# Performance work log

Measured on AMD Instinct MI355X. Metric: run time of the kernel, lower is better.

## Reference

```python
import jax, jax.numpy as jnp
import numpy as np

N_EMBD = 1024
HEAD_SIZE = 64  # n_embd // n_head = 1024 // 16


def setup_inputs() -> dict:
    key = jax.random.key(0)
    ks = jax.random.split(key, 7)
    B, T, C, H = 4, 2048, N_EMBD, HEAD_SIZE
    s = 1.0 / np.sqrt(C)
    return {
        "x": jax.random.normal(ks[0], (B, T, C), dtype=jnp.float32),
        "Wq": jax.random.normal(ks[1], (C, H), dtype=jnp.float32) * s,
        "bq": jax.random.normal(ks[2], (H,), dtype=jnp.float32) * 0.01,
        "Wk": jax.random.normal(ks[3], (C, H), dtype=jnp.float32) * s,
        "bk": jax.random.normal(ks[4], (H,), dtype=jnp.float32) * 0.01,
        "Wv": jax.random.normal(ks[5], (C, H), dtype=jnp.float32) * s,
        "bv": jax.random.normal(ks[6], (H,), dtype=jnp.float32) * 0.01,
    }


def reference(x, Wq, bq, Wk, bk, Wv, bv):
    # x: [B, T, C]
    B, T, C = x.shape
    q = x @ Wq + bq  # [B, T, H]
    k = x @ Wk + bk  # [B, T, H]
    v = x @ Wv + bv  # [B, T, H]
    # NOTE: original module does NOT scale by 1/sqrt(head_size)
    wei = jnp.einsum("bth,bsh->bts", q, k)  # [B, T, T]
    causal = jnp.tril(jnp.ones((T, T), dtype=bool))
    wei = jnp.where(causal, wei, -jnp.inf)
    wei = jax.nn.softmax(wei, axis=-1)
    out = jnp.einsum("bts,bsh->bth", wei, v)  # [B, T, H]
    return out
```

## Files before the change

### kernel.cpp

```cpp
#include <hip/hip_runtime.h>

typedef float f32x4 __attribute__((ext_vector_type(4)));
typedef short s16x4 __attribute__((ext_vector_type(4)));
typedef short s16x8 __attribute__((ext_vector_type(8)));

#define LOG2E 1.4426950408889634f

__device__ __forceinline__ short f2bf(float f) {
  unsigned u = __float_as_uint(f);
  unsigned r = (u + 0x7fffu + ((u >> 16) & 1u)) >> 16;
  return (short)r;
}
__device__ __forceinline__ float bf2f(short s) {
  return __uint_as_float(((unsigned)(unsigned short)s) << 16);
}
__device__ __forceinline__ unsigned cvt_pk_bf16(float a, float b) {
  unsigned r;
  asm("v_cvt_pk_bf16_f32 %0, %1, %2" : "=v"(r) : "v"(a), "v"(b));
  return r;
}

__device__ __forceinline__ f32x4 mfma16(s16x4 a, s16x4 b, f32x4 c) {
  return __builtin_amdgcn_mfma_f32_16x16x16bf16_1k(a, b, c, 0, 0, 0);
}
__device__ __forceinline__ f32x4 mfma32(s16x8 a, s16x8 b, f32x4 c) {
  return __builtin_amdgcn_mfma_f32_16x16x32_bf16(a, b, c, 0, 0, 0);
}

__device__ __forceinline__ void gl_lds16(const void* gp, void* sp) {
  __builtin_amdgcn_global_load_lds(
      (__attribute__((address_space(1))) void*)const_cast<void*>(gp),
      (__attribute__((address_space(3))) void*)sp, 16, 0, 0);
}

__global__ __launch_bounds__(256) void prep_w(
    const float* __restrict__ Wq, const float* __restrict__ Wk, const float* __restrict__ Wv,
    short* __restrict__ wt_hi, short* __restrict__ wt_lo) {
  int idx = blockIdx.x * 256 + threadIdx.x;
  int n = idx >> 10;
  int c = idx & 1023;
  const float* W = (n < 64) ? Wq : ((n < 128) ? Wk : Wv);
  float v = W[c * 64 + (n & 63)];
  short hi = f2bf(v);
  short lo = f2bf(v - bf2f(hi));
  wt_hi[idx] = hi;
  wt_lo[idx] = lo;
}

__global__ __launch_bounds__(512, 2) void proj_qkv(
    const float* __restrict__ x,
    const short* __restrict__ wt_hi, const short* __restrict__ wt_lo,
    const float* __restrict__ bq, const float* __restrict__ bk, const float* __restrict__ bv,
    short* __restrict__ q_hi, short* __restrict__ q_lo,
    short* __restrict__ k_hi, short* __restrict__ k_lo,
    short* __restrict__ v_t) {
  const int tid = threadIdx.x;
  const int lane = tid & 63;
  const int wv = tid >> 6;
  const int col = lane & 15;
  const int g = lane >> 4;
  const int mg = wv >> 2;
  const int ng = wv & 3;
  const int tokbase = blockIdx.x * 32;

  __shared__ short lds[5][12288];

  const int wsl = ((lane & 3) ^ ((lane >> 3) & 3)) * 8;
  const short* s0 = wt_hi + (size_t)(16 * wv + (lane >> 2)) * 1024 + wsl;
  const int d0 = wv * 512;
  const int c1 = wv + 8;
  const short* s1 = (c1 < 12 ? wt_hi + (size_t)(16 * c1 + (lane >> 2)) * 1024
                             : wt_lo + (size_t)(16 * (c1 - 12) + (lane >> 2)) * 1024) + wsl;
  const int d1 = (c1 < 12) ? c1 * 512 : 6144 + (c1 - 12) * 512;
  const int c2 = wv + 16;
  const bool isx = (c2 >= 20);
  const short* s2 = isx
      ? (const short*)(x + (size_t)(tokbase + 8 * (c2 - 20) + (lane >> 3)) * 1024 +
                       ((lane & 7) ^ (lane >> 3)) * 4)
      : wt_lo + (size_t)(16 * (c2 - 12) + (lane >> 2)) * 1024 + wsl;
  const int d2 = isx ? 10240 + (c2 - 20) * 512 : 6144 + (c2 - 12) * 512;
  const int st2 = isx ? 64 : 32;

#define STAGE(BP, S) do { \
    gl_lds16(s0 + (S) * 32, (BP) + d0); \
    gl_lds16(s1 + (S) * 32, (BP) + d1); \
    gl_lds16(s2 + (S) * st2, (BP) + d2); \
  } while (0)

#define PIPE_WAIT(N) do { \
    asm volatile("s_waitcnt vmcnt(" #N ")" ::: "memory"); \
    __builtin_amdgcn_s_barrier(); \
    __builtin_amdgcn_sched_barrier(0); \
  } while (0)
#define PIPE_END do { \
    asm volatile("s_waitcnt lgkmcnt(0)" ::: "memory"); \
    __builtin_amdgcn_sched_barrier(0); \
    __builtin_amdgcn_s_barrier(); \
  } while (0)

  const int arow = mg * 16 + col;
  const int xq0 = ((2 * g) ^ (arow & 7)) << 2;
  const int xq1 = ((2 * g + 1) ^ (arow & 7)) << 2;
  const int rq = ng * 16 + col;
  const int ws = (g ^ ((rq >> 1) & 3)) << 3;

  f32x4 accQ = {0,0,0,0}, accK = {0,0,0,0}, accV = {0,0,0,0};

  typedef union { unsigned u[4]; s16x8 v8; } pk8;

#define COMPUTE(BP) do { \
    const short* bp_ = (BP); \
    const float* xb_ = (const float*)(bp_ + 10240); \
    f32x4 x0_ = *(const f32x4*)(xb_ + arow * 32 + xq0); \
    f32x4 x1_ = *(const f32x4*)(xb_ + arow * 32 + xq1); \
    pk8 xh_, xl_; \
    xh_.u[0] = cvt_pk_bf16(x0_[0], x0_[1]); \
    xh_.u[1] = cvt_pk_bf16(x0_[2], x0_[3]); \
    xh_.u[2] = cvt_pk_bf16(x1_[0], x1_[1]); \
    xh_.u[3] = cvt_pk_bf16(x1_[2], x1_[3]); \
    xl_.u[0] = cvt_pk_bf16(x0_[0] - __uint_as_float(xh_.u[0] << 16), \
                           x0_[1] - __uint_as_float(xh_.u[0] & 0xffff0000u)); \
    xl_.u[1] = cvt_pk_bf16(x0_[2] - __uint_as_float(xh_.u[1] << 16), \
                           x0_[3] - __uint_as_float(xh_.u[1] & 0xffff0000u)); \
    xl_.u[2] = cvt_pk_bf16(x1_[0] - __uint_as_float(xh_.u[2] << 16), \
                           x1_[1] - __uint_as_float(xh_.u[2] & 0xffff0000u)); \
    xl_.u[3] = cvt_pk_bf16(x1_[2] - __uint_as_float(xh_.u[3] << 16), \
                           x1_[3] - __uint_as_float(xh_.u[3] & 0xffff0000u)); \
    s16x8 qh_ = *(const s16x8*)(bp_ + rq * 32 + ws); \
    s16x8 kh_ = *(const s16x8*)(bp_ + (64 + rq) * 32 + ws); \
    s16x8 vh_ = *(const s16x8*)(bp_ + (128 + rq) * 32 + ws); \
    s16x8 ql_ = *(const s16x8*)(bp_ + 6144 + rq * 32 + ws); \
    s16x8 kl_ = *(const s16x8*)(bp_ + 6144 + (64 + rq) * 32 + ws); \
    accQ = mfma32(xh_.v8, qh_, accQ); \
    accK = mfma32(xh_.v8, kh_, accK); \
    accV = mfma32(xh_.v8, vh_, accV); \
    accQ = mfma32(xl_.v8, qh_, accQ); \
    accK = mfma32(xl_.v8, kh_, accK); \
    accQ = mfma32(xh_.v8, ql_, accQ); \
    accK = mfma32(xh_.v8, kl_, accK); \
  } while (0)

  short* cA = &lds[0][0];
  short* cB = &lds[1][0];
  short* cC = &lds[2][0];
  short* cD = &lds[3][0];
  short* cE = &lds[4][0];

  STAGE(cA, 0); STAGE(cB, 1); STAGE(cC, 2); STAGE(cD, 3);

#pragma unroll 1
  for (int b = 0; b < 28; ++b) {
    STAGE(cE, b + 4);
    PIPE_WAIT(12);
    COMPUTE(cA);
    PIPE_END;
    short* t = cA; cA = cB; cB = cC; cC = cD; cD = cE; cE = t;
  }
  PIPE_WAIT(9); COMPUTE(cA); PIPE_END;
  PIPE_WAIT(6); COMPUTE(cB); PIPE_END;
  PIPE_WAIT(3); COMPUTE(cC); PIPE_END;
  PIPE_WAIT(0); COMPUTE(cD);

  {
    const int hQ = ng * 16 + col;
    const float biasq = bq[hQ];
    const float biask = bk[hQ];
    const float biasv = bv[hQ];
#pragma unroll
    for (int r = 0; r < 4; ++r) {
      const int tok = tokbase + mg * 16 + 4 * g + r;
      float fq = accQ[r] + biasq;
      short qh = f2bf(fq);
      q_hi[(size_t)tok * 64 + hQ] = qh;
      q_lo[(size_t)tok * 64 + hQ] = f2bf(fq - bf2f(qh));
      float fk = accK[r] + biask;
      short kh = f2bf(fk);
      k_hi[(size_t)tok * 64 + hQ] = kh;
      k_lo[(size_t)tok * 64 + hQ] = f2bf(fk - bf2f(kh));
      const int bb = tok >> 11;
      const int tl = tok & 2047;
      v_t[((size_t)bb * 64 + hQ) * 2048 + tl] = f2bf(accV[r] + biasv);
    }
  }
#undef STAGE
#undef PIPE_WAIT
#undef PIPE_END
#undef COMPUTE
}

__global__ __launch_bounds__(256, 3) void attn(
    const short* __restrict__ q_hi, const short* __restrict__ q_lo,
    const short* __restrict__ k_hi, const short* __restrict__ k_lo,
    const short* __restrict__ v_t,
    float* __restrict__ pm, float* __restrict__ pl, float* __restrict__ pO) {
  const int tid = threadIdx.x;
  const int lane = tid & 63;
  const int w = tid >> 6;
  const int col = lane & 15;
  const int g = lane >> 4;
  const int bid = blockIdx.x;
  const int p = bid & 31;
  const int b = (bid >> 5) & 3;
  const int s = bid >> 7;
  const int kb0 = 512 * s;
  if (kb0 > 64 * p + 63) return;
  const int S = (((64 * p + 63 - kb0) >> 5) + 1) < 16
                    ? (((64 * p + 63 - kb0) >> 5) + 1) : 16;

  __shared__ short lds[4][6144];

  const int qlo = 64 * p + 16 * w;

  const short* qbh = q_hi + (size_t)(b * 2048 + qlo + col) * 64 + g * 8;
  const short* qbl = q_lo + (size_t)(b * 2048 + qlo + col) * 64 + g * 8;
  s16x8 qh0 = *(const s16x8*)(qbh);
  s16x8 qh1 = *(const s16x8*)(qbh + 32);
  s16x8 ql0 = *(const s16x8*)(qbl);
  s16x8 ql1 = *(const s16x8*)(qbl + 32);
  asm volatile("s_waitcnt vmcnt(0)" ::: "memory");
  __builtin_amdgcn_sched_barrier(0);
  asm volatile("" : "+v"(qh0), "+v"(qh1), "+v"(ql0), "+v"(ql1));

  f32x4 o0 = {0,0,0,0}, o1 = {0,0,0,0}, o2 = {0,0,0,0}, o3 = {0,0,0,0};
  float m = -3.0e38f, l = 0.0f;

  const int kr32 = 8 * w + (lane >> 3);
  const int ksl = ((lane & 7) ^ (lane >> 3)) * 8;
  const short* khs = k_hi + (size_t)(b * 2048 + kb0 + kr32) * 64 + ksl;
  const short* kls = k_lo + (size_t)(b * 2048 + kb0 + kr32) * 64 + ksl;
  const int vh_r = 16 * w + (lane >> 2);
  const int vsl = ((2 * (lane & 3)) ^ (vh_r & 6)) * 4;
  const short* vs = v_t + ((size_t)b * 64 + vh_r) * 2048 + kb0 + vsl;
  const int kdst = kr32 * 64;
  const int vdst = 4096 + vh_r * 32 - (lane >> 2) * 32 + (lane & 15) * 8;

#define STAGE(J) do { \
    short* bp_ = &lds[(J) & 3][0]; \
    gl_lds16(khs + (J) * 32 * 64, bp_ + w * 512); \
    gl_lds16(kls + (J) * 32 * 64, bp_ + 2048 + w * 512); \
    gl_lds16(vs + (J) * 32, bp_ + 4096 + w * 512); \
  } while (0)

#define PIPE_WAIT(N) do { \
    asm volatile("s_waitcnt vmcnt(" #N ")" ::: "memory"); \
    __builtin_amdgcn_s_barrier(); \
    __builtin_amdgcn_sched_barrier(0); \
  } while (0)
#define PIPE_END do { \
    asm volatile("s_waitcnt lgkmcnt(0)" ::: "memory"); \
    __builtin_amdgcn_sched_barrier(0); \
    __builtin_amdgcn_s_barrier(); \
  } while (0)

  const int cx = col & 7;
  const int kslot0 = (g ^ cx) << 3;
  const int kslot1 = ((4 + g) ^ cx) << 3;
  const int vg0 = ((g) ^ (col & 6)) << 2;
  const int vg1 = ((4 + g) ^ (col & 6)) << 2;

#define SUBTILE(BP, KG0, VGOFF) do { \
    const short* kr_ = (BP) + ((KG0)&31) * 64 + col * 64; \
    s16x8 kh0_ = *(const s16x8*)(kr_ + kslot0); \
    s16x8 kh1_ = *(const s16x8*)(kr_ + kslot1); \
    s16x8 kl0_ = *(const s16x8*)(kr_ + 2048 + kslot0); \
    s16x8 kl1_ = *(const s16x8*)(kr_ + 2048 + kslot1); \
    f32x4 u1_ = {0,0,0,0}, u2_ = {0,0,0,0}; \
    u1_ = mfma32(kh0_, qh0, u1_); u1_ = mfma32(kh1_, qh1, u1_); \
    u2_ = mfma32(kh0_, ql0, u2_); u2_ = mfma32(kh1_, ql1, u2_); \
    u2_ = mfma32(kl0_, qh0, u2_); u2_ = mfma32(kl1_, qh1, u2_); \
    f32x4 s_ = u1_ + u2_; \
    if ((KG0) == qlo) { \
      _Pragma("unroll") for (int i = 0; i < 4; ++i) \
        if (4 * g + i > col) s_[i] = -3.0e38f; \
    } \
    float mx_ = fmaxf(fmaxf(s_[0], s_[1]), fmaxf(s_[2], s_[3])); \
    mx_ = fmaxf(mx_, __shfl_xor(mx_, 16)); \
    mx_ = fmaxf(mx_, __shfl_xor(mx_, 32)); \
    const float mn_ = fmaxf(m, mx_); \
    const float rs_ = __builtin_amdgcn_exp2f((m - mn_) * LOG2E); \
    const float p0_ = __builtin_amdgcn_exp2f((s_[0] - mn_) * LOG2E); \
    const float p1_ = __builtin_amdgcn_exp2f((s_[1] - mn_) * LOG2E); \
    const float p2_ = __builtin_amdgcn_exp2f((s_[2] - mn_) * LOG2E); \
    const float p3_ = __builtin_amdgcn_exp2f((s_[3] - mn_) * LOG2E); \
    l = l * rs_ + (p0_ + p1_ + p2_ + p3_); \
    o0 *= rs_; o1 *= rs_; o2 *= rs_; o3 *= rs_; \
    m = mn_; \
    s16x4 pb_; \
    pb_[0] = f2bf(p0_); pb_[1] = f2bf(p1_); pb_[2] = f2bf(p2_); pb_[3] = f2bf(p3_); \
    const short* vb_ = (BP) + 4096 + col * 32 + (VGOFF); \
    o0 = mfma16(*(const s16x4*)(vb_),        pb_, o0); \
    o1 = mfma16(*(const s16x4*)(vb_ + 512),  pb_, o1); \
    o2 = mfma16(*(const s16x4*)(vb_ + 1024), pb_, o2); \
    o3 = mfma16(*(const s16x4*)(vb_ + 1536), pb_, o3); \
  } while (0)

#define COMPUTE(J) do { \
    const int kb_ = kb0 + 32 * (J); \
    if (kb_ <= qlo + 15) { \
      short* bp_ = &lds[(J) & 3][0]; \
      SUBTILE(bp_, kb_, vg0); \
      if (kb_ + 16 <= qlo + 15) SUBTILE(bp_, kb_ + 16, vg1); \
    } \
  } while (0)

  STAGE(0); STAGE(1);
  if (S > 2) STAGE(2);

#pragma unroll 1
  for (int j = 0; j + 3 < S; ++j) {
    STAGE(j + 3);
    PIPE_WAIT(9);
    COMPUTE(j);
    PIPE_END;
  }
  if (S >= 3) { PIPE_WAIT(6); COMPUTE(S - 3); PIPE_END; }
  PIPE_WAIT(3); COMPUTE(S - 2); PIPE_END;
  PIPE_WAIT(0); COMPUTE(S - 1);

  l += __shfl_xor(l, 16);
  l += __shfl_xor(l, 32);
  const int row = b * 2048 + qlo + col;
  if (g == 0) {
    pm[s * 8192 + row] = m;
    pl[s * 8192 + row] = l;
  }
  {
    float* d = pO + ((size_t)s * 8192 + row) * 64 + 4 * g;
    *(f32x4*)(d)      = o0;
    *(f32x4*)(d + 16) = o1;
    *(f32x4*)(d + 32) = o2;
    *(f32x4*)(d + 48) = o3;
  }
#undef STAGE
#undef PIPE_WAIT
#undef PIPE_END
#undef SUBTILE
#undef COMPUTE
}

__global__ __launch_bounds__(256) void reduce_p(
    const float* __restrict__ pm, const float* __restrict__ pl,
    const float* __restrict__ pO, float* __restrict__ out) {
  const int idx = blockIdx.x * 256 + threadIdx.x;
  const int row = idx >> 4;
  const int hq = (idx & 15) * 4;
  const int smax = (row & 2047) >> 9;
  float M = -3.0e38f;
  for (int s = 0; s <= smax; ++s) M = fmaxf(M, pm[s * 8192 + row]);
  float L = 0.f;
  f32x4 acc = {0, 0, 0, 0};
  for (int s = 0; s <= smax; ++s) {
    const float ws = __builtin_amdgcn_exp2f((pm[s * 8192 + row] - M) * LOG2E);
    L += ws * pl[s * 8192 + row];
    f32x4 ov = *(const f32x4*)(pO + ((size_t)s * 8192 + row) * 64 + hq);
    acc += ov * ws;
  }
  const float invL = 1.0f / L;
  *(f32x4*)(out + (size_t)row * 64 + hq) = acc * invL;
}

extern "C" void kernel_launch(void* const* d_in, const int* in_sizes, int n_in,
                              void* d_out, int out_size, void* d_ws, size_t ws_size,
                              hipStream_t stream) {
  const float* x  = (const float*)d_in[0];
  const float* Wq = (const float*)d_in[1];
  const float* bq = (const float*)d_in[2];
  const float* Wk = (const float*)d_in[3];
  const float* bk = (const float*)d_in[4];
  const float* Wv = (const float*)d_in[5];
  const float* bv = (const float*)d_in[6];
  float* out = (float*)d_out;

  char* ws = (char*)d_ws;
  short* wt_hi = (short*)(ws);
  short* wt_lo = (short*)(ws + 393216);
  short* q_hi  = (short*)(ws + 786432);
  short* q_lo  = (short*)(ws + 786432 + 1048576);
  short* k_hi  = (short*)(ws + 786432 + 2 * 1048576);
  short* k_lo  = (short*)(ws + 786432 + 3 * 1048576);
  short* v_t   = (short*)(ws + 786432 + 4 * 1048576);
  float* pm    = (float*)(ws + 6029312);
  float* pl    = (float*)(ws + 6160384);
  float* pO    = (float*)(ws + 6291456);

  hipLaunchKernelGGL(prep_w, dim3(768), dim3(256), 0, stream, Wq, Wk, Wv, wt_hi, wt_lo);
  hipLaunchKernelGGL(proj_qkv, dim3(256), dim3(512), 0, stream,
                     x, wt_hi, wt_lo, bq, bk, bv, q_hi, q_lo, k_hi, k_lo, v_t);
  hipLaunchKernelGGL(attn, dim3(512), dim3(256), 0, stream,
                     q_hi, q_lo, k_hi, k_lo, v_t, pm, pl, pO);
  hipLaunchKernelGGL(reduce_p, dim3(512), dim3(256), 0, stream, pm, pl, pO, out);
}
```

Baseline: 54.60 us.

## Replace four-stage vmcnt-tracked K/V pipeline with syncthreads double buffering

The attention kernel's four-buffer LDS ring, driven by hand-placed s_waitcnt vmcnt counts and barriers, is replaced with a simple two-buffer scheme. Each iteration stages the next tile, computes the current one, and calls __syncthreads. This halves LDS per block and drops the occupancy hint in __launch_bounds__, which may let more blocks fit per CU. The trade-off is a prefetch depth of one tile. The barrier also likely drains all outstanding loads every iteration, so memory latency may be exposed rather than hidden.

```diff
diff --git a/kernel.cpp b/kernel.cpp
--- a/kernel.cpp
+++ b/kernel.cpp
@@ -188,7 +188,7 @@
 #undef COMPUTE
 }
 
-__global__ __launch_bounds__(256, 3) void attn(
+__global__ __launch_bounds__(256) void attn(
     const short* __restrict__ q_hi, const short* __restrict__ q_lo,
     const short* __restrict__ k_hi, const short* __restrict__ k_lo,
     const short* __restrict__ v_t,
@@ -207,7 +207,7 @@
   const int S = (((64 * p + 63 - kb0) >> 5) + 1) < 16
                     ? (((64 * p + 63 - kb0) >> 5) + 1) : 16;
 
-  __shared__ short lds[4][6144];
+  __shared__ short lds[2][6144];
 
   const int qlo = 64 * p + 16 * w;
 
@@ -217,8 +217,6 @@
   s16x8 qh1 = *(const s16x8*)(qbh + 32);
   s16x8 ql0 = *(const s16x8*)(qbl);
   s16x8 ql1 = *(const s16x8*)(qbl + 32);
-  asm volatile("s_waitcnt vmcnt(0)" ::: "memory");
-  __builtin_amdgcn_sched_barrier(0);
   asm volatile("" : "+v"(qh0), "+v"(qh1), "+v"(ql0), "+v"(ql1));
 
   f32x4 o0 = {0,0,0,0}, o1 = {0,0,0,0}, o2 = {0,0,0,0}, o3 = {0,0,0,0};
@@ -231,25 +229,12 @@
   const int vh_r = 16 * w + (lane >> 2);
   const int vsl = ((2 * (lane & 3)) ^ (vh_r & 6)) * 4;
   const short* vs = v_t + ((size_t)b * 64 + vh_r) * 2048 + kb0 + vsl;
-  const int kdst = kr32 * 64;
-  const int vdst = 4096 + vh_r * 32 - (lane >> 2) * 32 + (lane & 15) * 8;
 
 #define STAGE(J) do { \
-    short* bp_ = &lds[(J) & 3][0]; \
+    short* bp_ = &lds[(J) & 1][0]; \
     gl_lds16(khs + (J) * 32 * 64, bp_ + w * 512); \
     gl_lds16(kls + (J) * 32 * 64, bp_ + 2048 + w * 512); \
     gl_lds16(vs + (J) * 32, bp_ + 4096 + w * 512); \
-  } while (0)
-
-#define PIPE_WAIT(N) do { \
-    asm volatile("s_waitcnt vmcnt(" #N ")" ::: "memory"); \
-    __builtin_amdgcn_s_barrier(); \
-    __builtin_amdgcn_sched_barrier(0); \
-  } while (0)
-#define PIPE_END do { \
-    asm volatile("s_waitcnt lgkmcnt(0)" ::: "memory"); \
-    __builtin_amdgcn_sched_barrier(0); \
-    __builtin_amdgcn_s_barrier(); \
   } while (0)
 
   const int cx = col & 7;
@@ -297,25 +282,20 @@
 #define COMPUTE(J) do { \
     const int kb_ = kb0 + 32 * (J); \
     if (kb_ <= qlo + 15) { \
-      short* bp_ = &lds[(J) & 3][0]; \
+      const short* bp_ = &lds[(J) & 1][0]; \
       SUBTILE(bp_, kb_, vg0); \
       if (kb_ + 16 <= qlo + 15) SUBTILE(bp_, kb_ + 16, vg1); \
     } \
   } while (0)
 
-  STAGE(0); STAGE(1);
-  if (S > 2) STAGE(2);
-
+  STAGE(0);
+  __syncthreads();
 #pragma unroll 1
-  for (int j = 0; j + 3 < S; ++j) {
-    STAGE(j + 3);
-    PIPE_WAIT(9);
+  for (int j = 0; j < S; ++j) {
+    if (j + 1 < S) STAGE(j + 1);
     COMPUTE(j);
-    PIPE_END;
-  }
-  if (S >= 3) { PIPE_WAIT(6); COMPUTE(S - 3); PIPE_END; }
-  PIPE_WAIT(3); COMPUTE(S - 2); PIPE_END;
-  PIPE_WAIT(0); COMPUTE(S - 1);
+    __syncthreads();
+  }
 
   l += __shfl_xor(l, 16);
   l += __shfl_xor(l, 32);
@@ -332,8 +312,6 @@
     *(f32x4*)(d + 48) = o3;
   }
 #undef STAGE
-#undef PIPE_WAIT
-#undef PIPE_END
 #undef SUBTILE
 #undef COMPUTE
 }
```

New measurement: 57.57 us. 5.4% more time.
